# Kernel optimization log

Measured on AMD Instinct MI355X. Metric: run time of the kernel, lower is better.

Reference implementation:

```python
import jax, jax.numpy as jnp
import numpy as np

B, S, D = 2, 2048, 1024
H, HD = 16, 64

def setup_inputs() -> dict:
    key = jax.random.key(0)
    ks = jax.random.split(key, 5)
    scale = 1.0 / np.sqrt(D)
    x = jax.random.normal(ks[0], (B, S, D), dtype=jnp.float32)
    wq = jax.random.normal(ks[1], (D, H * HD), dtype=jnp.float32) * scale
    wk = jax.random.normal(ks[2], (D, H * HD), dtype=jnp.float32) * scale
    wv = jax.random.normal(ks[3], (D, H * HD), dtype=jnp.float32) * scale
    wo = jax.random.normal(ks[4], (H * HD, D), dtype=jnp.float32) * scale
    zeros = jnp.zeros((H * HD,), dtype=jnp.float32)
    return {"x": x, "wq": wq, "bq": zeros, "wk": wk, "bk": zeros,
            "wv": wv, "bv": zeros, "wo": wo, "bo": jnp.zeros((D,), jnp.float32)}

def reference(x, wq, bq, wk, bk, wv, bv, wo, bo):
    b, s, _ = x.shape
    att_scale = HD ** -0.5
    # QKV projections -> [b, h, s, hd]
    q = (x @ wq + bq).reshape(b, s, H, HD).transpose(0, 2, 1, 3)
    k = (x @ wk + bk).reshape(b, s, H, HD).transpose(0, 2, 1, 3)
    v = (x @ wv + bv).reshape(b, s, H, HD).transpose(0, 2, 1, 3)
    scores = jnp.einsum('bhqd,bhkd->bhqk', q, k) * att_scale
    weights = jax.nn.softmax(scores, axis=-1)
    out = jnp.einsum('bhqk,bhkd->bhqd', weights, v)
    out = out.transpose(0, 2, 1, 3).reshape(b, s, H * HD)
    return out @ wo + bo
```

## Files before the change

### kernel.cpp

```cpp
#include <hip/hip_runtime.h>
#include <hip/hip_bf16.h>

#define B_  2
#define S_  2048
#define D_  1024
#define H_  16
#define HD_ 64
#define M_  (B_*S_)

using bf16x8 = __attribute__((ext_vector_type(8))) short;
using f32x4  = __attribute__((ext_vector_type(4))) float;
using f32x16 = __attribute__((ext_vector_type(16))) float;
using u32x4  = __attribute__((ext_vector_type(4))) unsigned int;
using uint2v = __attribute__((ext_vector_type(2))) unsigned int;

static __device__ __forceinline__ ushort f2bf(float f) {
    __hip_bfloat16 h = __float2bfloat16(f);
    return *reinterpret_cast<ushort*>(&h);
}
static __device__ __forceinline__ float max3f(float a, float b, float c) {
    return fmaxf(fmaxf(a, b), c);
}
static __device__ __forceinline__ float fexp2(float x) {
#if __has_builtin(__builtin_amdgcn_exp2f)
    return __builtin_amdgcn_exp2f(x);
#else
    return exp2f(x);
#endif
}
static __device__ __forceinline__ unsigned int pack_bf16(float p0, float p1) {
    unsigned int a = __float_as_uint(p0), b = __float_as_uint(p1);
    a += 0x7fffu + ((a >> 16) & 1u);
    b += 0x7fffu + ((b >> 16) & 1u);
    return (a >> 16) | (b & 0xffff0000u);
}

#define GLDS16(gp, lp) __builtin_amdgcn_global_load_lds( \
    (const __attribute__((address_space(1))) void*)(gp), \
    (__attribute__((address_space(3))) void*)(lp), 16, 0, 0)

__global__ void convert_f32_bf16(const float* __restrict__ src, ushort* __restrict__ dst, int n) {
    int i = (blockIdx.x * blockDim.x + threadIdx.x) * 4;
    if (i < n) {
        float4 v = *reinterpret_cast<const float4*>(src + i);
        ushort4 o;
        o.x = f2bf(v.x); o.y = f2bf(v.y); o.z = f2bf(v.z); o.w = f2bf(v.w);
        *reinterpret_cast<ushort4*>(dst + i) = o;
    }
}

__global__ void transpose_w4(const float* __restrict__ wq, const float* __restrict__ wk,
                             const float* __restrict__ wv, const float* __restrict__ wo,
                             ushort* __restrict__ wqkvT, ushort* __restrict__ woT) {
    const int z = blockIdx.z;
    const float* src = (z == 0) ? wq : (z == 1) ? wk : (z == 2) ? wv : wo;
    ushort* dst = (z < 3) ? (wqkvT + (size_t)z * 1024 * 1024) : woT;
    const int R = 1024, C = 1024;
    __shared__ float t[32][33];
    int c0 = blockIdx.x * 32, r0 = blockIdx.y * 32;
    int tx = threadIdx.x, ty = threadIdx.y;
    #pragma unroll
    for (int i = 0; i < 4; i++)
        t[ty + i*8][tx] = src[(size_t)(r0 + ty + i*8) * C + c0 + tx];
    __syncthreads();
    #pragma unroll
    for (int i = 0; i < 4; i++)
        dst[(size_t)(c0 + ty + i*8) * R + r0 + tx] = f2bf(t[tx][ty + i*8]);
}

__global__ void transpose_v(const ushort* __restrict__ src, ushort* __restrict__ dst) {
    __shared__ ushort t[64][72];
    int bh = blockIdx.y, s0 = blockIdx.x * 64;
    #pragma unroll
    for (int p = 0; p < 2; p++) {
        int idx = threadIdx.x + p * 256;
        int r = idx >> 3, cu = (idx & 7) * 8;
        uint4 v = *reinterpret_cast<const uint4*>(src + (size_t)bh * 131072 + (size_t)(s0 + r) * 64 + cu);
        ushort tmp[8];
        *reinterpret_cast<uint4*>(tmp) = v;
        #pragma unroll
        for (int j = 0; j < 8; j++) t[cu + j][r] = tmp[j];
    }
    __syncthreads();
    #pragma unroll
    for (int p = 0; p < 2; p++) {
        int idx = threadIdx.x + p * 256;
        int r = idx >> 3, cu = (idx & 7) * 8;
        *reinterpret_cast<uint4*>(dst + (size_t)bh * 131072 + (size_t)r * S_ + s0 + cu) =
            *reinterpret_cast<uint4*>(&t[r][cu]);
    }
}

template<int MODE>
__launch_bounds__(256, 2)
__global__ void gemm_bt(const ushort* __restrict__ A, const ushort* __restrict__ Bt,
                        int Mdim, int Ndim, int Kdim,
                        ushort* __restrict__ qout, ushort* __restrict__ kout, ushort* __restrict__ vout,
                        const float* __restrict__ bq, const float* __restrict__ bk, const float* __restrict__ bv,
                        float* __restrict__ out, const float* __restrict__ bias)
{
    __shared__ __align__(16) ushort As[128][64];
    __shared__ __align__(16) ushort Bs[128][64];
    const int tid  = threadIdx.x;
    const int lane = tid & 63, wave = tid >> 6;
    const int wm = wave & 1, wn = wave >> 1;
    const int lin = blockIdx.x;
    const int xcd = lin & 7, idx = lin >> 3;
    int my, nx;
    if (MODE == 0) { my = (xcd >> 1) * 8 + idx / 12; nx = (xcd & 1) * 12 + idx % 12; }
    else           { my = xcd * 4 + (idx >> 3);      nx = idx & 7; }
    const int m0 = my * 128, n0 = nx * 128;
    const int g = lane >> 4, c = lane & 15;

    f32x4 acc[4][4];
    #pragma unroll
    for (int i = 0; i < 4; i++)
        #pragma unroll
        for (int j = 0; j < 4; j++) acc[i][j] = (f32x4){0.f, 0.f, 0.f, 0.f};

    const int arow  = lane >> 3;
    const int aslot = (lane & 7) ^ arow;
    const ushort* Ag = A  + (size_t)(m0 + arow) * Kdim + aslot * 8;
    const ushort* Bg = Bt + (size_t)(n0 + arow) * Kdim + aslot * 8;

    #pragma unroll 1
    for (int kt = 0; kt < Kdim; kt += 64) {
        #pragma unroll
        for (int p = 0; p < 4; p++) {
            int ch = wave + p * 4;
            GLDS16(Ag + (size_t)(ch*8) * Kdim + kt, &As[ch*8][0]);
            GLDS16(Bg + (size_t)(ch*8) * Kdim + kt, &Bs[ch*8][0]);
        }
        __syncthreads();
        #pragma unroll
        for (int ks = 0; ks < 2; ks++) {
            bf16x8 af[4], bfr[4];
            #pragma unroll
            for (int t = 0; t < 4; t++) {
                int sl = ((ks*4 + g) ^ (c & 7)) * 8;
                af[t]  = *reinterpret_cast<const bf16x8*>(&As[wm*64 + t*16 + c][sl]);
                bfr[t] = *reinterpret_cast<const bf16x8*>(&Bs[wn*64 + t*16 + c][sl]);
            }
            #pragma unroll
            for (int i = 0; i < 4; i++)
                #pragma unroll
                for (int j = 0; j < 4; j++)
                    acc[i][j] = __builtin_amdgcn_mfma_f32_16x16x32_bf16(af[i], bfr[j], acc[i][j], 0, 0, 0);
        }
        __syncthreads();
    }

    const float qscale = 0.125f * 1.4426950408889634f;
    if (MODE == 0) {
        const int which = n0 >> 10;
        const int cc0 = (n0 & 1023) + wn*64;
        const int h = cc0 >> 6;
        ushort* dst0 = (which == 0) ? qout : (which == 1) ? kout : vout;
        const float* bp = (which == 0) ? bq : (which == 1) ? bk : bv;
        const float scl = (which == 0) ? qscale : 1.f;
        float bj[4];
        #pragma unroll
        for (int j = 0; j < 4; j++) bj[j] = bp[cc0 + j*16 + c];
        #pragma unroll
        for (int i = 0; i < 4; i++) {
            #pragma unroll
            for (int r = 0; r < 4; r++) {
                int row = m0 + wm*64 + i*16 + g*4 + r;
                int b = row >> 11, s = row & 2047;
                ushort* orow = dst0 + (((size_t)(b*H_ + h)) * S_ + s) * HD_;
                #pragma unroll
                for (int j = 0; j < 4; j++)
                    orow[j*16 + c] = f2bf((acc[i][j][r] + bj[j]) * scl);
            }
        }
    } else {
        float bj[4];
        #pragma unroll
        for (int j = 0; j < 4; j++) bj[j] = bias[n0 + wn*64 + j*16 + c];
        #pragma unroll
        for (int i = 0; i < 4; i++)
            #pragma unroll
            for (int r = 0; r < 4; r++) {
                int row = m0 + wm*64 + i*16 + g*4 + r;
                float* orow = out + (size_t)row * Ndim + n0 + wn*64;
                #pragma unroll
                for (int j = 0; j < 4; j++)
                    orow[j*16 + c] = acc[i][j][r] + bj[j];
            }
    }
}

__launch_bounds__(512, 4)
__global__ void attn_kernel(const ushort* __restrict__ Q, const ushort* __restrict__ K,
                            const ushort* __restrict__ Vt, ushort* __restrict__ O)
{
    __shared__ __align__(16) ushort Ks[2][2][64][64];
    __shared__ __align__(16) ushort Vs[2][2][64][64];
    const int tid = threadIdx.x, lane = tid & 63, w = tid >> 6;
    const int grp = w >> 2, wq4 = w & 3;
    const int q31 = lane & 31, hi = lane >> 5, x7 = lane & 7;

    int lin = blockIdx.x + gridDim.x * blockIdx.y;
    int xcd = lin & 7, idx = lin >> 3;
    int bh = xcd * 4 + (idx & 3);
    int qb = idx >> 2;
    const int q0 = qb * 128;
    const int kt_base = grp * 1024;
    const ushort* Kp = K  + (size_t)bh * S_ * HD_;
    const ushort* Vp = Vt + (size_t)bh * HD_ * S_;

    bf16x8 qf[4];
    #pragma unroll
    for (int c4 = 0; c4 < 4; c4++)
        qf[c4] = *reinterpret_cast<const bf16x8*>(
            Q + (size_t)bh * S_ * HD_ + (size_t)(q0 + wq4*32 + q31) * HD_ + c4*16 + hi*8);

    f32x16 acc0, acc1;
    #pragma unroll
    for (int r = 0; r < 16; r++) { acc0[r] = 0.f; acc1[r] = 0.f; }
    float m_i = -INFINITY, l_i = 0.f;

    const int srow  = lane >> 3;
    const int sslot = (lane & 7) ^ srow;
    const ushort* kg = Kp + (size_t)srow * HD_ + sslot * 8;
    const ushort* vg = Vp + (size_t)srow * S_  + sslot * 8;

    auto stage = [&](int buf, int kt) {
        #pragma unroll
        for (int p = 0; p < 2; p++) {
            int ch = wq4 + p * 4;
            GLDS16(kg + (size_t)(kt + ch*8) * HD_, &Ks[grp][buf][ch*8][0]);
            GLDS16(vg + (size_t)(ch*8) * S_ + kt,  &Vs[grp][buf][ch*8][0]);
        }
    };

    auto softmax_pack = [&](const f32x16& st, bf16x8& pf0, bf16x8& pf1) {
        float g0 = max3f(st[0],  st[1],  st[2]);
        float g1 = max3f(st[3],  st[4],  st[5]);
        float g2 = max3f(st[6],  st[7],  st[8]);
        float g3 = max3f(st[9],  st[10], st[11]);
        float g4 = max3f(st[12], st[13], st[14]);
        float pm = fmaxf(max3f(g0, g1, g2), max3f(g3, g4, st[15]));
#if __has_builtin(__builtin_amdgcn_permlane32_swap)
        {
            uint2v r = __builtin_amdgcn_permlane32_swap(__float_as_uint(pm), __float_as_uint(pm), false, false);
            pm = fmaxf(__uint_as_float(r.x), __uint_as_float(r.y));
        }
#else
        pm = fmaxf(pm, __shfl_xor(pm, 32));
#endif
        if (__any(pm > m_i + 8.f)) {
            float mnew = fmaxf(m_i, pm);
            float al = fexp2(m_i - mnew);
            l_i *= al;
            #pragma unroll
            for (int r = 0; r < 16; r++) { acc0[r] *= al; acc1[r] *= al; }
            m_i = mnew;
        }
        float rs = 0.f;
        unsigned int dd[8];
        #pragma unroll
        for (int r2 = 0; r2 < 8; r2++) {
            float p0 = fexp2(st[r2*2]     - m_i);
            float p1 = fexp2(st[r2*2 + 1] - m_i);
            rs += p0 + p1;
            dd[r2] = pack_bf16(p0, p1);
        }
#if __has_builtin(__builtin_amdgcn_permlane32_swap)
        {
            uint2v r = __builtin_amdgcn_permlane32_swap(__float_as_uint(rs), __float_as_uint(rs), false, false);
            rs = __uint_as_float(r.x) + __uint_as_float(r.y);
        }
#else
        rs += __shfl_xor(rs, 32);
#endif
        l_i += rs;
        u32x4 t0, t1;
#if __has_builtin(__builtin_amdgcn_permlane32_swap)
        {
            uint2v s02 = __builtin_amdgcn_permlane32_swap(dd[0], dd[2], false, false);
            uint2v s13 = __builtin_amdgcn_permlane32_swap(dd[1], dd[3], false, false);
            uint2v s46 = __builtin_amdgcn_permlane32_swap(dd[4], dd[6], false, false);
            uint2v s57 = __builtin_amdgcn_permlane32_swap(dd[5], dd[7], false, false);
            t0 = (u32x4){s02.x, s13.x, s02.y, s13.y};
            t1 = (u32x4){s46.x, s57.x, s46.y, s57.y};
        }
#else
        {
            unsigned int ee[8];
            #pragma unroll
            for (int r2 = 0; r2 < 8; r2++)
                ee[r2] = (unsigned int)__shfl_xor((int)dd[r2], 32);
            t0 = (u32x4){ hi ? ee[2] : dd[0], hi ? ee[3] : dd[1],
                          hi ? dd[2] : ee[0], hi ? dd[3] : ee[1] };
            t1 = (u32x4){ hi ? ee[6] : dd[4], hi ? ee[7] : dd[5],
                          hi ? dd[6] : ee[4], hi ? dd[7] : ee[5] };
        }
#endif
        pf0 = *reinterpret_cast<bf16x8*>(&t0);
        pf1 = *reinterpret_cast<bf16x8*>(&t1);
    };

    auto compute64 = [&](int buf) {
        const ushort (*ks)[64] = Ks[grp][buf];
        const ushort (*vs)[64] = Vs[grp][buf];
        f32x16 st0, st1;
        #pragma unroll
        for (int r = 0; r < 16; r++) { st0[r] = 0.f; st1[r] = 0.f; }
        __builtin_amdgcn_s_setprio(1);
        #pragma unroll
        for (int c4 = 0; c4 < 4; c4++) {
            bf16x8 kf = *reinterpret_cast<const bf16x8*>(&ks[q31][((c4*2 + hi) ^ x7) * 8]);
            st0 = __builtin_amdgcn_mfma_f32_32x32x16_bf16(kf, qf[c4], st0, 0, 0, 0);
        }
        #pragma unroll
        for (int c4 = 0; c4 < 4; c4++) {
            bf16x8 kf = *reinterpret_cast<const bf16x8*>(&ks[32 + q31][((c4*2 + hi) ^ x7) * 8]);
            st1 = __builtin_amdgcn_mfma_f32_32x32x16_bf16(kf, qf[c4], st1, 0, 0, 0);
        }
        __builtin_amdgcn_s_setprio(0);

        bf16x8 pf0, pf1;
        softmax_pack(st0, pf0, pf1);
        {
            bf16x8 vf0 = *reinterpret_cast<const bf16x8*>(&vs[q31]     [((0 + hi) ^ x7) * 8]);
            bf16x8 vf1 = *reinterpret_cast<const bf16x8*>(&vs[q31]     [((2 + hi) ^ x7) * 8]);
            bf16x8 vf2 = *reinterpret_cast<const bf16x8*>(&vs[32 + q31][((0 + hi) ^ x7) * 8]);
            bf16x8 vf3 = *reinterpret_cast<const bf16x8*>(&vs[32 + q31][((2 + hi) ^ x7) * 8]);
            __builtin_amdgcn_s_setprio(1);
            acc0 = __builtin_amdgcn_mfma_f32_32x32x16_bf16(vf0, pf0, acc0, 0, 0, 0);
            acc0 = __builtin_amdgcn_mfma_f32_32x32x16_bf16(vf1, pf1, acc0, 0, 0, 0);
            acc1 = __builtin_amdgcn_mfma_f32_32x32x16_bf16(vf2, pf0, acc1, 0, 0, 0);
            acc1 = __builtin_amdgcn_mfma_f32_32x32x16_bf16(vf3, pf1, acc1, 0, 0, 0);
            __builtin_amdgcn_s_setprio(0);
        }
        softmax_pack(st1, pf0, pf1);
        {
            bf16x8 vf0 = *reinterpret_cast<const bf16x8*>(&vs[q31]     [((4 + hi) ^ x7) * 8]);
            bf16x8 vf1 = *reinterpret_cast<const bf16x8*>(&vs[q31]     [((6 + hi) ^ x7) * 8]);
            bf16x8 vf2 = *reinterpret_cast<const bf16x8*>(&vs[32 + q31][((4 + hi) ^ x7) * 8]);
            bf16x8 vf3 = *reinterpret_cast<const bf16x8*>(&vs[32 + q31][((6 + hi) ^ x7) * 8]);
            __builtin_amdgcn_s_setprio(1);
            acc0 = __builtin_amdgcn_mfma_f32_32x32x16_bf16(vf0, pf0, acc0, 0, 0, 0);
            acc0 = __builtin_amdgcn_mfma_f32_32x32x16_bf16(vf1, pf1, acc0, 0, 0, 0);
            acc1 = __builtin_amdgcn_mfma_f32_32x32x16_bf16(vf2, pf0, acc1, 0, 0, 0);
            acc1 = __builtin_amdgcn_mfma_f32_32x32x16_bf16(vf3, pf1, acc1, 0, 0, 0);
            __builtin_amdgcn_s_setprio(0);
        }
    };

    stage(0, kt_base);
    __syncthreads();
    #pragma unroll 1
    for (int it = 0; it < 15; ++it) {
        stage((it & 1) ^ 1, kt_base + (it + 1) * 64);
        compute64(it & 1);
        __syncthreads();
    }
    compute64(1);

    __syncthreads();
    float* fb = (wq4 < 2) ? reinterpret_cast<float*>(&Ks[0][0][0][0])
                          : reinterpret_cast<float*>(&Vs[0][0][0][0]);
    const int slot = ((wq4 & 1) * 64 + lane) * 35;
    if (grp == 1) {
        #pragma unroll
        for (int r = 0; r < 16; r++) { fb[slot + r] = acc0[r]; fb[slot + 16 + r] = acc1[r]; }
        fb[slot + 32] = m_i;
        fb[slot + 33] = l_i;
    }
    __syncthreads();
    if (grp == 0) {
        float m2 = fb[slot + 32], l2 = fb[slot + 33];
        float mm = fmaxf(m_i, m2);
        float a1 = fexp2(m_i - mm), a2 = fexp2(m2 - mm);
        float inv = 1.f / (l_i * a1 + l2 * a2);
        const int b = bh >> 4, h = bh & 15;
        const int s = q0 + wq4*32 + q31;
        ushort* op = O + (size_t)(b*S_ + s) * 1024 + h*64;
        #pragma unroll
        for (int rg = 0; rg < 4; rg++) {
            int hd0 = rg*8 + hi*4;
            ushort4 o;
            o.x = f2bf((acc0[rg*4+0]*a1 + fb[slot + rg*4+0]*a2) * inv);
            o.y = f2bf((acc0[rg*4+1]*a1 + fb[slot + rg*4+1]*a2) * inv);
            o.z = f2bf((acc0[rg*4+2]*a1 + fb[slot + rg*4+2]*a2) * inv);
            o.w = f2bf((acc0[rg*4+3]*a1 + fb[slot + rg*4+3]*a2) * inv);
            *reinterpret_cast<ushort4*>(op + hd0) = o;
            o.x = f2bf((acc1[rg*4+0]*a1 + fb[slot + 16 + rg*4+0]*a2) * inv);
            o.y = f2bf((acc1[rg*4+1]*a1 + fb[slot + 16 + rg*4+1]*a2) * inv);
            o.z = f2bf((acc1[rg*4+2]*a1 + fb[slot + 16 + rg*4+2]*a2) * inv);
            o.w = f2bf((acc1[rg*4+3]*a1 + fb[slot + 16 + rg*4+3]*a2) * inv);
            *reinterpret_cast<ushort4*>(op + 32 + hd0) = o;
        }
    }
}

extern "C" void kernel_launch(void* const* d_in, const int* in_sizes, int n_in,
                              void* d_out, int out_size, void* d_ws, size_t ws_size,
                              hipStream_t stream)
{
    const float* x  = (const float*)d_in[0];
    const float* wq = (const float*)d_in[1];
    const float* bq = (const float*)d_in[2];
    const float* wk = (const float*)d_in[3];
    const float* bk = (const float*)d_in[4];
    const float* wv = (const float*)d_in[5];
    const float* bv = (const float*)d_in[6];
    const float* wo = (const float*)d_in[7];
    const float* bo = (const float*)d_in[8];
    float* out = (float*)d_out;

    char* ws = (char*)d_ws;
    ushort* xb    = (ushort*)(ws);
    ushort* wqkvT = (ushort*)(ws + (8ull  << 20));
    ushort* woT   = (ushort*)(ws + (14ull << 20));
    ushort* qw    = (ushort*)(ws + (16ull << 20));
    ushort* kw    = (ushort*)(ws + (24ull << 20));
    ushort* vw    = (ushort*)(ws + (32ull << 20));
    ushort* ao    = (ushort*)(ws + (40ull << 20));
    ushort* vtw   = xb;

    convert_f32_bf16<<<4096, 256, 0, stream>>>(x, xb, M_ * D_);
    transpose_w4<<<dim3(32, 32, 4), dim3(32, 8), 0, stream>>>(wq, wk, wv, wo, wqkvT, woT);

    gemm_bt<0><<<768, 256, 0, stream>>>(xb, wqkvT, M_, 3072, 1024,
                                        qw, kw, vw, bq, bk, bv, nullptr, nullptr);
    transpose_v<<<dim3(32, 32), 256, 0, stream>>>(vw, vtw);
    attn_kernel<<<dim3(16, 32), 512, 0, stream>>>(qw, kw, vtw, ao);
    gemm_bt<1><<<256, 256, 0, stream>>>(ao, woT, M_, 1024, 1024,
                                        nullptr, nullptr, nullptr, nullptr, nullptr, nullptr,
                                        out, bo);
}
```

Baseline: 204.8 us.

## Fuse prep kernels, write V transposed in GEMM epilogue, retile output GEMM

Merges the x conversion and weight transposes into one prep launch. The QKV GEMM now writes V directly in transposed [hd][s] layout, which removes the separate transpose_v kernel and its round trip through memory. The output projection GEMM uses a 128x64 tile with 512 blocks instead of 128x128 with 256, giving more blocks to fill the CUs. Launch bounds are raised to 3 blocks per CU. The transposed V stores are strided 8-byte writes, which may coalesce worse than the old row writes.

```diff
diff --git a/kernel.cpp b/kernel.cpp
--- a/kernel.cpp
+++ b/kernel.cpp
@@ -39,20 +39,24 @@
     (const __attribute__((address_space(1))) void*)(gp), \
     (__attribute__((address_space(3))) void*)(lp), 16, 0, 0)
 
-__global__ void convert_f32_bf16(const float* __restrict__ src, ushort* __restrict__ dst, int n) {
-    int i = (blockIdx.x * blockDim.x + threadIdx.x) * 4;
-    if (i < n) {
-        float4 v = *reinterpret_cast<const float4*>(src + i);
-        ushort4 o;
-        o.x = f2bf(v.x); o.y = f2bf(v.y); o.z = f2bf(v.z); o.w = f2bf(v.w);
-        *reinterpret_cast<ushort4*>(dst + i) = o;
-    }
-}
-
-__global__ void transpose_w4(const float* __restrict__ wq, const float* __restrict__ wk,
-                             const float* __restrict__ wv, const float* __restrict__ wo,
-                             ushort* __restrict__ wqkvT, ushort* __restrict__ woT) {
+__global__ void prep(const float* __restrict__ x,
+                     const float* __restrict__ wq, const float* __restrict__ wk,
+                     const float* __restrict__ wv, const float* __restrict__ wo,
+                     ushort* __restrict__ xb, ushort* __restrict__ wqkvT, ushort* __restrict__ woT) {
     const int z = blockIdx.z;
+    if (z == 4) {
+        int blk = blockIdx.y * 32 + blockIdx.x;
+        int tid = threadIdx.y * 32 + threadIdx.x;
+        #pragma unroll
+        for (int q = 0; q < 4; q++) {
+            int i = ((q * 1024 + blk) * 256 + tid) * 4;
+            float4 v = *reinterpret_cast<const float4*>(x + i);
+            ushort4 o;
+            o.x = f2bf(v.x); o.y = f2bf(v.y); o.z = f2bf(v.z); o.w = f2bf(v.w);
+            *reinterpret_cast<ushort4*>(xb + i) = o;
+        }
+        return;
+    }
     const float* src = (z == 0) ? wq : (z == 1) ? wk : (z == 2) ? wv : wo;
     ushort* dst = (z < 3) ? (wqkvT + (size_t)z * 1024 * 1024) : woT;
     const int R = 1024, C = 1024;
@@ -68,39 +72,17 @@
         dst[(size_t)(c0 + ty + i*8) * R + r0 + tx] = f2bf(t[tx][ty + i*8]);
 }
 
-__global__ void transpose_v(const ushort* __restrict__ src, ushort* __restrict__ dst) {
-    __shared__ ushort t[64][72];
-    int bh = blockIdx.y, s0 = blockIdx.x * 64;
-    #pragma unroll
-    for (int p = 0; p < 2; p++) {
-        int idx = threadIdx.x + p * 256;
-        int r = idx >> 3, cu = (idx & 7) * 8;
-        uint4 v = *reinterpret_cast<const uint4*>(src + (size_t)bh * 131072 + (size_t)(s0 + r) * 64 + cu);
-        ushort tmp[8];
-        *reinterpret_cast<uint4*>(tmp) = v;
-        #pragma unroll
-        for (int j = 0; j < 8; j++) t[cu + j][r] = tmp[j];
-    }
-    __syncthreads();
-    #pragma unroll
-    for (int p = 0; p < 2; p++) {
-        int idx = threadIdx.x + p * 256;
-        int r = idx >> 3, cu = (idx & 7) * 8;
-        *reinterpret_cast<uint4*>(dst + (size_t)bh * 131072 + (size_t)r * S_ + s0 + cu) =
-            *reinterpret_cast<uint4*>(&t[r][cu]);
-    }
-}
-
-template<int MODE>
-__launch_bounds__(256, 2)
+template<int MODE, int NJ>
+__launch_bounds__(256, 3)
 __global__ void gemm_bt(const ushort* __restrict__ A, const ushort* __restrict__ Bt,
                         int Mdim, int Ndim, int Kdim,
                         ushort* __restrict__ qout, ushort* __restrict__ kout, ushort* __restrict__ vout,
                         const float* __restrict__ bq, const float* __restrict__ bk, const float* __restrict__ bv,
                         float* __restrict__ out, const float* __restrict__ bias)
 {
+    constexpr int BN = NJ * 32;
     __shared__ __align__(16) ushort As[128][64];
-    __shared__ __align__(16) ushort Bs[128][64];
+    __shared__ __align__(16) ushort Bs[BN][64];
     const int tid  = threadIdx.x;
     const int lane = tid & 63, wave = tid >> 6;
     const int wm = wave & 1, wn = wave >> 1;
@@ -108,15 +90,15 @@
     const int xcd = lin & 7, idx = lin >> 3;
     int my, nx;
     if (MODE == 0) { my = (xcd >> 1) * 8 + idx / 12; nx = (xcd & 1) * 12 + idx % 12; }
-    else           { my = xcd * 4 + (idx >> 3);      nx = idx & 7; }
-    const int m0 = my * 128, n0 = nx * 128;
+    else           { my = xcd * 4 + (idx >> 4);      nx = idx & 15; }
+    const int m0 = my * 128, n0 = nx * BN;
     const int g = lane >> 4, c = lane & 15;
 
-    f32x4 acc[4][4];
+    f32x4 acc[4][NJ];
     #pragma unroll
     for (int i = 0; i < 4; i++)
         #pragma unroll
-        for (int j = 0; j < 4; j++) acc[i][j] = (f32x4){0.f, 0.f, 0.f, 0.f};
+        for (int j = 0; j < NJ; j++) acc[i][j] = (f32x4){0.f, 0.f, 0.f, 0.f};
 
     const int arow  = lane >> 3;
     const int aslot = (lane & 7) ^ arow;
@@ -129,22 +111,30 @@
         for (int p = 0; p < 4; p++) {
             int ch = wave + p * 4;
             GLDS16(Ag + (size_t)(ch*8) * Kdim + kt, &As[ch*8][0]);
+        }
+        #pragma unroll
+        for (int p = 0; p < NJ; p++) {
+            int ch = wave + p * 4;
             GLDS16(Bg + (size_t)(ch*8) * Kdim + kt, &Bs[ch*8][0]);
         }
         __syncthreads();
         #pragma unroll
         for (int ks = 0; ks < 2; ks++) {
-            bf16x8 af[4], bfr[4];
+            bf16x8 af[4], bfr[NJ];
             #pragma unroll
             for (int t = 0; t < 4; t++) {
                 int sl = ((ks*4 + g) ^ (c & 7)) * 8;
-                af[t]  = *reinterpret_cast<const bf16x8*>(&As[wm*64 + t*16 + c][sl]);
-                bfr[t] = *reinterpret_cast<const bf16x8*>(&Bs[wn*64 + t*16 + c][sl]);
+                af[t] = *reinterpret_cast<const bf16x8*>(&As[wm*64 + t*16 + c][sl]);
+            }
+            #pragma unroll
+            for (int t = 0; t < NJ; t++) {
+                int sl = ((ks*4 + g) ^ (c & 7)) * 8;
+                bfr[t] = *reinterpret_cast<const bf16x8*>(&Bs[wn*(NJ*16) + t*16 + c][sl]);
             }
             #pragma unroll
             for (int i = 0; i < 4; i++)
                 #pragma unroll
-                for (int j = 0; j < 4; j++)
+                for (int j = 0; j < NJ; j++)
                     acc[i][j] = __builtin_amdgcn_mfma_f32_16x16x32_bf16(af[i], bfr[j], acc[i][j], 0, 0, 0);
         }
         __syncthreads();
@@ -155,36 +145,59 @@
         const int which = n0 >> 10;
         const int cc0 = (n0 & 1023) + wn*64;
         const int h = cc0 >> 6;
-        ushort* dst0 = (which == 0) ? qout : (which == 1) ? kout : vout;
-        const float* bp = (which == 0) ? bq : (which == 1) ? bk : bv;
-        const float scl = (which == 0) ? qscale : 1.f;
-        float bj[4];
-        #pragma unroll
-        for (int j = 0; j < 4; j++) bj[j] = bp[cc0 + j*16 + c];
-        #pragma unroll
-        for (int i = 0; i < 4; i++) {
+        const int b = m0 >> 11;
+        if (which == 2) {
+            float bj[4];
+            #pragma unroll
+            for (int j = 0; j < 4; j++) bj[j] = bv[cc0 + j*16 + c];
+            const int sbase = (m0 & 2047) + wm*64 + g*4;
+            ushort* vb = vout + (size_t)(b*H_ + h) * HD_ * S_;
+            #pragma unroll
+            for (int i = 0; i < 4; i++) {
+                int s0 = sbase + i*16;
+                #pragma unroll
+                for (int j = 0; j < 4; j++) {
+                    int hd = j*16 + c;
+                    ushort4 o;
+                    o.x = f2bf(acc[i][j][0] + bj[j]);
+                    o.y = f2bf(acc[i][j][1] + bj[j]);
+                    o.z = f2bf(acc[i][j][2] + bj[j]);
+                    o.w = f2bf(acc[i][j][3] + bj[j]);
+                    *reinterpret_cast<ushort4*>(vb + (size_t)hd * S_ + s0) = o;
+                }
+            }
+        } else {
+            ushort* dst0 = (which == 0) ? qout : kout;
+            const float* bp = (which == 0) ? bq : bk;
+            const float scl = (which == 0) ? qscale : 1.f;
+            float bj[4];
+            #pragma unroll
+            for (int j = 0; j < 4; j++) bj[j] = bp[cc0 + j*16 + c];
+            #pragma unroll
+            for (int i = 0; i < 4; i++) {
+                #pragma unroll
+                for (int r = 0; r < 4; r++) {
+                    int row = m0 + wm*64 + i*16 + g*4 + r;
+                    int s = row & 2047;
+                    ushort* orow = dst0 + (((size_t)(b*H_ + h)) * S_ + s) * HD_;
+                    #pragma unroll
+                    for (int j = 0; j < 4; j++)
+                        orow[j*16 + c] = f2bf((acc[i][j][r] + bj[j]) * scl);
+                }
+            }
+        }
+    } else {
+        float bj[NJ];
+        #pragma unroll
+        for (int j = 0; j < NJ; j++) bj[j] = bias[n0 + wn*(NJ*16) + j*16 + c];
+        #pragma unroll
+        for (int i = 0; i < 4; i++)
             #pragma unroll
             for (int r = 0; r < 4; r++) {
                 int row = m0 + wm*64 + i*16 + g*4 + r;
-                int b = row >> 11, s = row & 2047;
-                ushort* orow = dst0 + (((size_t)(b*H_ + h)) * S_ + s) * HD_;
+                float* orow = out + (size_t)row * Ndim + n0 + wn*(NJ*16);
                 #pragma unroll
-                for (int j = 0; j < 4; j++)
-                    orow[j*16 + c] = f2bf((acc[i][j][r] + bj[j]) * scl);
-            }
-        }
-    } else {
-        float bj[4];
-        #pragma unroll
-        for (int j = 0; j < 4; j++) bj[j] = bias[n0 + wn*64 + j*16 + c];
-        #pragma unroll
-        for (int i = 0; i < 4; i++)
-            #pragma unroll
-            for (int r = 0; r < 4; r++) {
-                int row = m0 + wm*64 + i*16 + g*4 + r;
-                float* orow = out + (size_t)row * Ndim + n0 + wn*64;
-                #pragma unroll
-                for (int j = 0; j < 4; j++)
+                for (int j = 0; j < NJ; j++)
                     orow[j*16 + c] = acc[i][j][r] + bj[j];
             }
     }
@@ -417,18 +430,15 @@
     ushort* woT   = (ushort*)(ws + (14ull << 20));
     ushort* qw    = (ushort*)(ws + (16ull << 20));
     ushort* kw    = (ushort*)(ws + (24ull << 20));
-    ushort* vw    = (ushort*)(ws + (32ull << 20));
+    ushort* vtw   = (ushort*)(ws + (32ull << 20));
     ushort* ao    = (ushort*)(ws + (40ull << 20));
-    ushort* vtw   = xb;
-
-    convert_f32_bf16<<<4096, 256, 0, stream>>>(x, xb, M_ * D_);
-    transpose_w4<<<dim3(32, 32, 4), dim3(32, 8), 0, stream>>>(wq, wk, wv, wo, wqkvT, woT);
-
-    gemm_bt<0><<<768, 256, 0, stream>>>(xb, wqkvT, M_, 3072, 1024,
-                                        qw, kw, vw, bq, bk, bv, nullptr, nullptr);
-    transpose_v<<<dim3(32, 32), 256, 0, stream>>>(vw, vtw);
+
+    prep<<<dim3(32, 32, 5), dim3(32, 8), 0, stream>>>(x, wq, wk, wv, wo, xb, wqkvT, woT);
+
+    gemm_bt<0, 4><<<768, 256, 0, stream>>>(xb, wqkvT, M_, 3072, 1024,
+                                           qw, kw, vtw, bq, bk, bv, nullptr, nullptr);
     attn_kernel<<<dim3(16, 32), 512, 0, stream>>>(qw, kw, vtw, ao);
-    gemm_bt<1><<<256, 256, 0, stream>>>(ao, woT, M_, 1024, 1024,
-                                        nullptr, nullptr, nullptr, nullptr, nullptr, nullptr,
-                                        out, bo);
-}
+    gemm_bt<1, 2><<<512, 256, 0, stream>>>(ao, woT, M_, 1024, 1024,
+                                           nullptr, nullptr, nullptr, nullptr, nullptr, nullptr,
+                                           out, bo);
+}
```

Measured after the change: 193.1 us, median of 3. -5.7%, faster.
